# Optimization experiments

Hardware: AMD Instinct MI355X
Metric: run time of the kernel (lower is better)

The kernel has to match this reference:

```python
import jax, jax.numpy as jnp
import numpy as np

IN_DIM, H_DIM, OUT_DIM, N_LAYERS = 512, 1024, 512, 2


def _linear_params(key, out_d, in_d, bias=True):
    k1, k2 = jax.random.split(key)
    bound = 1.0 / np.sqrt(in_d)
    W = jax.random.uniform(k1, (out_d, in_d), jnp.float32, -bound, bound)
    if bias:
        b = jax.random.uniform(k2, (out_d,), jnp.float32, -bound, bound)
        return W, b
    return (W,)


def setup_inputs() -> dict:
    key = jax.random.key(0)
    keys = jax.random.split(key, 32)
    inp = {"x": jax.random.normal(keys[0], (32, 512, IN_DIM), jnp.float32)}
    ki = 1
    for layer in range(N_LAYERS):
        lin = IN_DIM if layer == 0 else H_DIM
        for gate in ("z", "r", "g"):
            W, b = _linear_params(keys[ki], H_DIM, lin); ki += 1
            inp[f"Wx{gate}{layer}"] = W
            inp[f"bx{gate}{layer}"] = b
            (Wh,) = _linear_params(keys[ki], H_DIM, H_DIM, bias=False); ki += 1
            inp[f"Wh{gate}{layer}"] = Wh
    Why, bhy = _linear_params(keys[ki], OUT_DIM, H_DIM)
    inp["Why"] = Why
    inp["bhy"] = bhy
    return inp


def _gru_forward(x, layers, Why, bhy):
    B = x.shape[0]
    h0 = tuple(jnp.zeros((B, H_DIM), x.dtype) for _ in range(N_LAYERS))

    def cell(p, h_prev, xin):
        Wxz, bxz, Whz, Wxr, bxr, Whr, Wxg, bxg, Whg = p
        z = jax.nn.sigmoid(xin @ Wxz.T + bxz + h_prev @ Whz.T)
        r = jax.nn.sigmoid(xin @ Wxr.T + bxr + h_prev @ Whr.T)
        g = jnp.tanh(xin @ Wxg.T + bxg + (r * h_prev) @ Whg.T)
        return z * h_prev + (1.0 - z) * g

    def step(hs, xt):
        cur = xt
        new_hs = []
        for p, h in zip(layers, hs):
            h_new = cell(p, h, cur)
            new_hs.append(h_new)
            cur = h_new
        yt = cur @ Why.T + bhy  # (B, O)
        return tuple(new_hs), yt

    xs = jnp.swapaxes(x, 0, 1)  # (S, B, I)
    final_hs, ys = jax.lax.scan(step, h0, xs)
    layer_output = jnp.swapaxes(ys, 0, 1)  # (B, S, O)
    hidden_state = jnp.stack(final_hs, axis=1)  # (B, L, H)
    return layer_output, hidden_state


def reference(x,
              Wxz0, bxz0, Whz0, Wxr0, bxr0, Whr0, Wxg0, bxg0, Whg0,
              Wxz1, bxz1, Whz1, Wxr1, bxr1, Whr1, Wxg1, bxg1, Whg1,
              Why, bhy):
    layers = [
        (Wxz0, bxz0, Whz0, Wxr0, bxr0, Whr0, Wxg0, bxg0, Whg0),
        (Wxz1, bxz1, Whz1, Wxr1, bxr1, Whr1, Wxg1, bxg1, Whg1),
    ]
    return _gru_forward(x, layers, Why, bhy)
```

## Files before the change

### kernel.cpp

```cpp
#include <hip/hip_runtime.h>

#define SS 512
#define NWG 52
#define NTHR 512
#define OUT_HID_OFF 8388608

typedef _Float16 fh8 __attribute__((ext_vector_type(8)));
typedef float f32x4 __attribute__((ext_vector_type(4)));

struct GP {
  const float *x;
  const float *Wxz0,*bxz0,*Whz0,*Wxr0,*bxr0,*Whr0,*Wxg0,*bxg0,*Whg0;
  const float *Wxz1,*bxz1,*Whz1,*Wxr1,*bxr1,*Whr1,*Wxg1,*bxg1,*Whg1;
  const float *Why,*bhy;
  float *out;
  _Float16 *xb;
  _Float16 *wzr0,*wzr1,*wg0,*wg1,*wy;
  float *h0f,*h1f;
  _Float16 *h0h,*h1h;
  float *z0,*z1;
  _Float16 *r0,*r1;
  unsigned *fg0,*fg1;
  unsigned *fzr0,*fzr1;
  unsigned *fy;
};

__device__ __forceinline__ void astore(float* p, float v) {
  __hip_atomic_store(p, v, __ATOMIC_RELAXED, __HIP_MEMORY_SCOPE_AGENT);
}
__device__ __forceinline__ void bload(uint4& d, const void* p) {
  asm volatile("global_load_dwordx4 %0, %1, off sc0 sc1"
               : "=&v"(d) : "v"(p) : "memory");
}
__device__ __forceinline__ void bload1(float& d, const float* p) {
  asm volatile("global_load_dword %0, %1, off sc0 sc1"
               : "=&v"(d) : "v"(p) : "memory");
}
__device__ __forceinline__ void sstore(_Float16* pd, float v) {
  _Float16 h = (_Float16)v;
  unsigned short u; __builtin_memcpy(&u, &h, 2);
  asm volatile("global_store_short %0, %1, off sc0 sc1"
               :: "v"(pd), "v"((unsigned)u) : "memory");
}
__device__ __forceinline__ fh8 u2h(uint4 v){ fh8 r; __builtin_memcpy(&r, &v, 16); return r; }
__device__ __forceinline__ uint4 h2u(fh8 v){ uint4 r; __builtin_memcpy(&r, &v, 16); return r; }
__device__ __forceinline__ float sigmf(float v){ return 1.f/(1.f+__expf(-v)); }

__global__ __launch_bounds__(256) void pack(GP p) {
  const long gid = (long)blockIdx.x*256 + threadIdx.x;
  if (gid < 1441792) {
    long u; int KC; _Float16* dst;
    if (gid < 393216)       { u=gid;         KC=48; dst=p.wzr0; }
    else if (gid < 917504)  { u=gid-393216;  KC=64; dst=p.wzr1; }
    else if (gid < 1114112) { u=gid-917504;  KC=48; dst=p.wg0;  }
    else if (gid < 1376256) { u=gid-1114112; KC=64; dst=p.wg1;  }
    else                    { u=gid-1376256; KC=32; dst=p.wy;   }
    const int per = KC*64;
    const int ntg = (int)(u/per); const int r = (int)(u%per);
    const int kc = r>>6, lane = r&63;
    const int n = ntg*16 + (lane&15);
    const int k = kc*32 + ((lane>>4)<<3);
    const float* src;
    if (gid < 393216) {
      int g = n>>10, nn = n&1023;
      src = (k<512) ? ((g?p.Wxr0:p.Wxz0) + (size_t)nn*512 + k)
                    : ((g?p.Whr0:p.Whz0) + (size_t)nn*1024 + (k-512));
    } else if (gid < 917504) {
      int g = n>>10, nn = n&1023;
      src = (k<1024) ? ((g?p.Wxr1:p.Wxz1) + (size_t)nn*1024 + k)
                     : ((g?p.Whr1:p.Whz1) + (size_t)nn*1024 + (k-1024));
    } else if (gid < 1114112) {
      src = (k<512) ? (p.Wxg0 + (size_t)n*512 + k)
                    : (p.Whg0 + (size_t)n*1024 + (k-512));
    } else if (gid < 1376256) {
      src = (k<1024) ? (p.Wxg1 + (size_t)n*1024 + k)
                     : (p.Whg1 + (size_t)n*1024 + (k-1024));
    } else {
      src = p.Why + (size_t)n*1024 + k;
    }
    float4 f0 = *(const float4*)src, f1 = *(const float4*)(src+4);
    fh8 h;
    h[0]=(_Float16)f0.x; h[1]=(_Float16)f0.y; h[2]=(_Float16)f0.z; h[3]=(_Float16)f0.w;
    h[4]=(_Float16)f1.x; h[5]=(_Float16)f1.y; h[6]=(_Float16)f1.z; h[7]=(_Float16)f1.w;
    *(fh8*)(dst + u*8) = h;
  } else if (gid < 2490368) {
    const long e = (gid - 1441792)*8;
    float4 f0 = *(const float4*)(p.x + e), f1 = *(const float4*)(p.x + e + 4);
    fh8 h;
    h[0]=(_Float16)f0.x; h[1]=(_Float16)f0.y; h[2]=(_Float16)f0.z; h[3]=(_Float16)f0.w;
    h[4]=(_Float16)f1.x; h[5]=(_Float16)f1.y; h[6]=(_Float16)f1.z; h[7]=(_Float16)f1.w;
    *(fh8*)(p.xb + e) = h;
  }
}

__device__ __forceinline__ void waitf(const unsigned* fb, int n, int need) {
  if (need > 0) {
    if ((int)threadIdx.x < n) {
      const unsigned* f = fb + (size_t)threadIdx.x*32;
      while ((int)__hip_atomic_load(f, __ATOMIC_RELAXED, __HIP_MEMORY_SCOPE_AGENT) < need)
        __builtin_amdgcn_s_sleep(1);
    }
    asm volatile("" ::: "memory");
    __syncthreads();
  }
}
__device__ __forceinline__ void setflag(unsigned* f, unsigned v) {
  asm volatile("s_waitcnt vmcnt(0) lgkmcnt(0)" ::: "memory");
  __syncthreads();
  if (threadIdx.x == 0)
    __hip_atomic_store(f, v, __ATOMIC_RELAXED, __HIP_MEMORY_SCOPE_AGENT);
}

__device__ __forceinline__ void issue_copy(uint4* R, const _Float16* base, int row, int s16) {
  const char* sp = (const char*)(base + (size_t)row*1024) + s16*64;
  bload(R[0], sp); bload(R[1], sp+16); bload(R[2], sp+32); bload(R[3], sp+48);
}
__device__ __forceinline__ void issue_prod(uint4* Ra, uint4* Rh,
    const _Float16* ra, const _Float16* ha, int row, int s16) {
  const char* rp = (const char*)(ra + (size_t)row*1024) + s16*64;
  const char* hp = (const char*)(ha + (size_t)row*1024) + s16*64;
  #pragma unroll
  for (int q = 0; q < 4; ++q) { bload(Ra[q], rp + q*16); bload(Rh[q], hp + q*16); }
}
__device__ __forceinline__ void issue_x(uint4* R, const _Float16* xab, int row, int s16) {
  const uint4* sp = (const uint4*)(xab + (size_t)row*262144 + (size_t)s16*32);
  R[0]=sp[0]; R[1]=sp[1]; R[2]=sp[2]; R[3]=sp[3];
}
__device__ __forceinline__ void commit4(const uint4* R, char* As, int s, int row, int s16) {
  const int key = (row & 15) << 4;
  char* d = As + (size_t)row*4096;
  const int kb0 = s*1024 + s16*64;
  #pragma unroll
  for (int q = 0; q < 4; ++q) *(uint4*)(d + ((kb0 + q*16) ^ key)) = R[q];
}
__device__ __forceinline__ void commit_prod(const uint4* Ra, const uint4* Rh,
    char* As, int s, int row, int s16) {
  const int key = (row & 15) << 4;
  char* d = As + (size_t)row*4096;
  const int kb0 = s*1024 + s16*64;
  #pragma unroll
  for (int q = 0; q < 4; ++q) {
    fh8 o = u2h(Ra[q]) * u2h(Rh[q]);
    *(uint4*)(d + ((kb0 + q*16) ^ key)) = h2u(o);
  }
}

__device__ __forceinline__ void sweep_range(const char* As, const _Float16* wpk,
    int ntg, int KC, int k0, int k1, int l, f32x4& acc0, f32x4& acc1) {
  const int lrow = l & 15, key = lrow << 4, lg16 = (l >> 4) << 4;
  const char* ab = As + (size_t)lrow*4096;
  const _Float16* wb = wpk + (size_t)ntg*KC*512 + (size_t)l*8;
  #pragma unroll 8
  for (int kk = k0; kk < k1; ++kk) {
    const int off = (kk*64 + lg16) ^ key;
    fh8 a0 = *(const fh8*)(ab + off);
    fh8 a1 = *(const fh8*)(ab + 16*4096 + off);
    fh8 b  = *(const fh8*)(wb + (size_t)kk*512);
    acc0 = __builtin_amdgcn_mfma_f32_16x16x32_f16(a0, b, acc0, 0, 0, 0);
    acc1 = __builtin_amdgcn_mfma_f32_16x16x32_f16(a1, b, acc1, 0, 0, 0);
  }
}

__device__ __forceinline__ void epi_zr(const f32x4& a0, const f32x4& a1, int ntg, int l,
    const float* bz, const float* br, float* zbuf, _Float16* rbuf) {
  const int col = (ntg << 4) | (l & 15);
  const int gate = col >> 10, cc = col & 1023;
  const float bias = gate ? br[cc] : bz[cc];
  const int brow = (l >> 4) << 2;
  #pragma unroll
  for (int q = 0; q < 4; ++q) {
    const float v0 = sigmf(a0[q]+bias), v1 = sigmf(a1[q]+bias);
    if (gate) {
      sstore(rbuf + (size_t)(brow+q)*1024 + cc, v0);
      sstore(rbuf + (size_t)(brow+q+16)*1024 + cc, v1);
    } else {
      astore(zbuf + (size_t)(brow+q)*1024 + cc, v0);
      astore(zbuf + (size_t)(brow+q+16)*1024 + cc, v1);
    }
  }
}

__global__ __launch_bounds__(NTHR, 2) void gru_main(GP p) {
  __shared__ char As[131072];
  const int tid = threadIdx.x, wg = blockIdx.x;
  const int wid = tid >> 6, l = tid & 63;
  const int row = tid >> 4, s16 = tid & 15;
  const int brow = (l >> 4) << 2;

  if (wg < 16) {
    const int ntg = wg*8 + wid;
    for (int t = 0; t < SS; ++t) {
      { uint4 Rx[4];
        issue_x(Rx, p.xb + (size_t)t*512, row, s16);
        commit4(Rx, As, 0, row, s16); }
      __syncthreads();
      f32x4 a0 = {0.f,0.f,0.f,0.f}, a1 = {0.f,0.f,0.f,0.f};
      sweep_range(As, p.wzr0, ntg, 48, 0, 16, l, a0, a1);
      waitf(p.fg0, 8, t);
      { const _Float16* hb = p.h0h + (size_t)((t-1)&3)*32768;
        uint4 R0[4], R1[4];
        issue_copy(R0, hb, row, s16);
        issue_copy(R1, hb+512, row, s16);
        asm volatile("s_waitcnt vmcnt(0)" ::: "memory");
        __builtin_amdgcn_sched_barrier(0);
        commit4(R0, As, 1, row, s16);
        commit4(R1, As, 2, row, s16); }
      __syncthreads();
      sweep_range(As, p.wzr0, ntg, 48, 16, 48, l, a0, a1);
      epi_zr(a0, a1, ntg, l, p.bxz0, p.bxr0,
             p.z0 + (size_t)(t&1)*32768, p.r0 + (size_t)(t&1)*32768);
      setflag(p.fzr0 + (size_t)wg*32, (unsigned)(t+1));
    }
  } else if (wg < 32) {
    const int ntg = (wg-16)*8 + wid;
    for (int t = 0; t < SS; ++t) {
      waitf(p.fg0, 8, t+1);
      { const _Float16* hb = p.h0h + (size_t)(t&3)*32768;
        uint4 R0[4], R1[4];
        issue_copy(R0, hb, row, s16);
        issue_copy(R1, hb+512, row, s16);
        asm volatile("s_waitcnt vmcnt(0)" ::: "memory");
        __builtin_amdgcn_sched_barrier(0);
        commit4(R0, As, 0, row, s16);
        commit4(R1, As, 1, row, s16); }
      __syncthreads();
      f32x4 a0 = {0.f,0.f,0.f,0.f}, a1 = {0.f,0.f,0.f,0.f};
      sweep_range(As, p.wzr1, ntg, 64, 0, 32, l, a0, a1);
      waitf(p.fg1, 8, t);
      { const _Float16* hb = p.h1h + (size_t)((t-1)&3)*32768;
        uint4 R0[4], R1[4];
        issue_copy(R0, hb, row, s16);
        issue_copy(R1, hb+512, row, s16);
        asm volatile("s_waitcnt vmcnt(0)" ::: "memory");
        __builtin_amdgcn_sched_barrier(0);
        commit4(R0, As, 2, row, s16);
        commit4(R1, As, 3, row, s16); }
      __syncthreads();
      sweep_range(As, p.wzr1, ntg, 64, 32, 64, l, a0, a1);
      epi_zr(a0, a1, ntg, l, p.bxz1, p.bxr1,
             p.z1 + (size_t)(t&1)*32768, p.r1 + (size_t)(t&1)*32768);
      setflag(p.fzr1 + (size_t)(wg-16)*32, (unsigned)(t+1));
    }
  } else if (wg < 40) {
    const int gi = wg - 32;
    const int ntg = gi*8 + wid;
    const int colB = (ntg << 4) | (l & 15);
    const float biasB = p.bxg0[colB];
    float hv[8];
    #pragma unroll
    for (int q = 0; q < 8; ++q) hv[q] = 0.f;
    for (int u = 0; u < SS; ++u) {
      { uint4 Rx[4];
        issue_x(Rx, p.xb + (size_t)u*512, row, s16);
        commit4(Rx, As, 0, row, s16); }
      __syncthreads();
      f32x4 a0 = {0.f,0.f,0.f,0.f}, a1 = {0.f,0.f,0.f,0.f};
      sweep_range(As, p.wg0, ntg, 48, 0, 16, l, a0, a1);
      waitf(p.fzr0, 16, u+1);
      waitf(p.fg0,  8,  u);
      waitf(p.fzr1, 16, u-3);
      waitf(p.fg1,  8,  u-3);
      { const float*    zr = p.z0 + (size_t)(u&1)*32768;
        const _Float16* rr = p.r0 + (size_t)(u&1)*32768;
        const _Float16* hh = p.h0h + (size_t)((u-1)&3)*32768;
        float zv[8];
        uint4 Ra[8], Rh[8];
        issue_prod(&Ra[0], &Rh[0], rr, hh, row, s16);
        issue_prod(&Ra[4], &Rh[4], rr+512, hh+512, row, s16);
        #pragma unroll
        for (int q = 0; q < 4; ++q) {
          bload1(zv[q],   zr + (size_t)(brow+q)*1024 + colB);
          bload1(zv[4+q], zr + (size_t)(brow+q+16)*1024 + colB);
        }
        asm volatile("s_waitcnt vmcnt(0)" ::: "memory");
        __builtin_amdgcn_sched_barrier(0);
        commit_prod(&Ra[0], &Rh[0], As, 1, row, s16);
        commit_prod(&Ra[4], &Rh[4], As, 2, row, s16);
        __syncthreads();
        sweep_range(As, p.wg0, ntg, 48, 16, 48, l, a0, a1);
        float* hF = p.h0f + (size_t)(u&3)*32768;
        _Float16* hH = p.h0h + (size_t)(u&3)*32768;
        #pragma unroll
        for (int q = 0; q < 4; ++q) {
          { const float g = tanhf(a0[q]+biasB);
            const float hn = zv[q]*hv[q] + (1.f-zv[q])*g;
            hv[q] = hn;
            astore(hF + (size_t)(brow+q)*1024 + colB, hn);
            sstore(hH + (size_t)(brow+q)*1024 + colB, hn); }
          { const float g = tanhf(a1[q]+biasB);
            const float hn = zv[4+q]*hv[4+q] + (1.f-zv[4+q])*g;
            hv[4+q] = hn;
            astore(hF + (size_t)(brow+q+16)*1024 + colB, hn);
            sstore(hH + (size_t)(brow+q+16)*1024 + colB, hn); }
        }
      }
      setflag(p.fg0 + (size_t)gi*32, (unsigned)(u+1));
    }
    #pragma unroll
    for (int q = 0; q < 4; ++q) {
      p.out[OUT_HID_OFF + (size_t)(brow+q)*2048 + colB]    = hv[q];
      p.out[OUT_HID_OFF + (size_t)(brow+q+16)*2048 + colB] = hv[4+q];
    }
  } else if (wg < 48) {
    const int gi = wg - 40;
    const int ntg = gi*8 + wid;
    const int colB = (ntg << 4) | (l & 15);
    const float biasB = p.bxg1[colB];
    float hv[8];
    #pragma unroll
    for (int q = 0; q < 8; ++q) hv[q] = 0.f;
    for (int v = 0; v < SS; ++v) {
      waitf(p.fg0, 8, v+1);
      { const _Float16* hb = p.h0h + (size_t)(v&3)*32768;
        uint4 R0[4], R1[4];
        issue_copy(R0, hb, row, s16);
        issue_copy(R1, hb+512, row, s16);
        asm volatile("s_waitcnt vmcnt(0)" ::: "memory");
        __builtin_amdgcn_sched_barrier(0);
        commit4(R0, As, 0, row, s16);
        commit4(R1, As, 1, row, s16); }
      __syncthreads();
      f32x4 a0 = {0.f,0.f,0.f,0.f}, a1 = {0.f,0.f,0.f,0.f};
      sweep_range(As, p.wg1, ntg, 64, 0, 32, l, a0, a1);
      waitf(p.fzr1, 16, v+1);
      waitf(p.fg1,  8,  v);
      waitf(p.fy,   4,  v-3);
      { const float*    zr = p.z1 + (size_t)(v&1)*32768;
        const _Float16* rr = p.r1 + (size_t)(v&1)*32768;
        const _Float16* hh = p.h1h + (size_t)((v-1)&3)*32768;
        float zv[8];
        uint4 Ra[8], Rh[8];
        issue_prod(&Ra[0], &Rh[0], rr, hh, row, s16);
        issue_prod(&Ra[4], &Rh[4], rr+512, hh+512, row, s16);
        #pragma unroll
        for (int q = 0; q < 4; ++q) {
          bload1(zv[q],   zr + (size_t)(brow+q)*1024 + colB);
          bload1(zv[4+q], zr + (size_t)(brow+q+16)*1024 + colB);
        }
        asm volatile("s_waitcnt vmcnt(0)" ::: "memory");
        __builtin_amdgcn_sched_barrier(0);
        commit_prod(&Ra[0], &Rh[0], As, 2, row, s16);
        commit_prod(&Ra[4], &Rh[4], As, 3, row, s16);
        __syncthreads();
        sweep_range(As, p.wg1, ntg, 64, 32, 64, l, a0, a1);
        float* hF = p.h1f + (size_t)(v&3)*32768;
        _Float16* hH = p.h1h + (size_t)(v&3)*32768;
        #pragma unroll
        for (int q = 0; q < 4; ++q) {
          { const float g = tanhf(a0[q]+biasB);
            const float hn = zv[q]*hv[q] + (1.f-zv[q])*g;
            hv[q] = hn;
            astore(hF + (size_t)(brow+q)*1024 + colB, hn);
            sstore(hH + (size_t)(brow+q)*1024 + colB, hn); }
          { const float g = tanhf(a1[q]+biasB);
            const float hn = zv[4+q]*hv[4+q] + (1.f-zv[4+q])*g;
            hv[4+q] = hn;
            astore(hF + (size_t)(brow+q+16)*1024 + colB, hn);
            sstore(hH + (size_t)(brow+q+16)*1024 + colB, hn); }
        }
      }
      setflag(p.fg1 + (size_t)gi*32, (unsigned)(v+1));
    }
    #pragma unroll
    for (int q = 0; q < 4; ++q) {
      p.out[OUT_HID_OFF + (size_t)(brow+q)*2048 + 1024 + colB]    = hv[q];
      p.out[OUT_HID_OFF + (size_t)(brow+q+16)*2048 + 1024 + colB] = hv[4+q];
    }
  } else {
    const int ntg = (wg-48)*8 + wid;
    const int col = (ntg << 4) | (l & 15);
    const float bias = p.bhy[col];
    for (int w = 0; w < SS; ++w) {
      waitf(p.fg1, 8, w+1);
      { const _Float16* hb = p.h1h + (size_t)(w&3)*32768;
        uint4 R0[4], R1[4];
        issue_copy(R0, hb, row, s16);
        issue_copy(R1, hb+512, row, s16);
        asm volatile("s_waitcnt vmcnt(0)" ::: "memory");
        __builtin_amdgcn_sched_barrier(0);
        commit4(R0, As, 0, row, s16);
        commit4(R1, As, 1, row, s16); }
      __syncthreads();
      f32x4 a0 = {0.f,0.f,0.f,0.f}, a1 = {0.f,0.f,0.f,0.f};
      sweep_range(As, p.wy, ntg, 32, 0, 32, l, a0, a1);
      #pragma unroll
      for (int q = 0; q < 4; ++q) {
        p.out[(size_t)(brow+q)*262144    + (size_t)w*512 + col] = a0[q] + bias;
        p.out[(size_t)(brow+q+16)*262144 + (size_t)w*512 + col] = a1[q] + bias;
      }
      setflag(p.fy + (size_t)(wg-48)*32, (unsigned)(w+1));
    }
  }
}

extern "C" void kernel_launch(void* const* d_in, const int* in_sizes, int n_in,
                              void* d_out, int out_size, void* d_ws, size_t ws_size,
                              hipStream_t stream) {
  GP P;
  P.x    = (const float*)d_in[0];
  P.Wxz0 = (const float*)d_in[1];  P.bxz0 = (const float*)d_in[2];  P.Whz0 = (const float*)d_in[3];
  P.Wxr0 = (const float*)d_in[4];  P.bxr0 = (const float*)d_in[5];  P.Whr0 = (const float*)d_in[6];
  P.Wxg0 = (const float*)d_in[7];  P.bxg0 = (const float*)d_in[8];  P.Whg0 = (const float*)d_in[9];
  P.Wxz1 = (const float*)d_in[10]; P.bxz1 = (const float*)d_in[11]; P.Whz1 = (const float*)d_in[12];
  P.Wxr1 = (const float*)d_in[13]; P.bxr1 = (const float*)d_in[14]; P.Whr1 = (const float*)d_in[15];
  P.Wxg1 = (const float*)d_in[16]; P.bxg1 = (const float*)d_in[17]; P.Whg1 = (const float*)d_in[18];
  P.Why  = (const float*)d_in[19]; P.bhy  = (const float*)d_in[20];
  P.out  = (float*)d_out;

  char* ws = (char*)d_ws;
  P.xb   = (_Float16*)(ws + 0);
  P.wzr0 = (_Float16*)(ws + 16777216);
  P.wzr1 = (_Float16*)(ws + 23068672);
  P.wg0  = (_Float16*)(ws + 31457280);
  P.wg1  = (_Float16*)(ws + 34603008);
  P.wy   = (_Float16*)(ws + 38797312);
  P.h0f  = (float*)   (ws + 39845888);
  P.h1f  = (float*)   (ws + 40370176);
  P.h0h  = (_Float16*)(ws + 40894464);
  P.h1h  = (_Float16*)(ws + 41156608);
  P.z0   = (float*)   (ws + 41418752);
  P.z1   = (float*)   (ws + 41680896);
  P.r0   = (_Float16*)(ws + 41943040);
  P.r1   = (_Float16*)(ws + 42074112);
  P.fg0  = (unsigned*)(ws + 42205184);
  P.fg1  = (unsigned*)(ws + 42206208);
  P.fzr0 = (unsigned*)(ws + 42207232);
  P.fzr1 = (unsigned*)(ws + 42209280);
  P.fy   = (unsigned*)(ws + 42211328);

  hipMemsetAsync(ws + 39845888, 0, 42213888 - 39845888, stream);

  pack<<<dim3(9728), dim3(256), 0, stream>>>(P);

  void* args[] = { &P };
  hipError_t err = hipLaunchCooperativeKernel((const void*)gru_main,
                                              dim3(NWG), dim3(NTHR), args, 0, stream);
  if (err != hipSuccess) {
    (void)hipGetLastError();
    gru_main<<<dim3(NWG), dim3(NTHR), 0, stream>>>(P);
  }
}
```

Measured before the change: 7.825 ms.

## Split recurrent GRU work across 100 workgroups with half-batch tiles and paired stores

Each workgroup now handles 4 column tiles. Each wave computes a 16-row half of the batch instead of both halves, so the zr and g stages use twice as many workgroups (NWG goes from 52 to 100). Per-element fp16 and fp32 stores are replaced by lane-pair shuffles and 32/64-bit atomic stores, and multiple flag waits are merged into one concurrent poll. The aim is to shorten the per-timestep critical path by spreading the MFMA sweeps over more CUs, at the cost of more flags to poll and more cross-workgroup synchronization.

```diff
diff --git a/kernel.cpp b/kernel.cpp
--- a/kernel.cpp
+++ b/kernel.cpp
@@ -1,7 +1,7 @@
 #include <hip/hip_runtime.h>
 
 #define SS 512
-#define NWG 52
+#define NWG 100
 #define NTHR 512
 #define OUT_HID_OFF 8388608
 
@@ -25,7 +25,16 @@
   unsigned *fy;
 };
 
-__device__ __forceinline__ void astore(float* p, float v) {
+__device__ __forceinline__ void astoref(float* p, float v) {
+  __hip_atomic_store(p, v, __ATOMIC_RELAXED, __HIP_MEMORY_SCOPE_AGENT);
+}
+__device__ __forceinline__ void astore2f(float* p, float a, float b) {
+  unsigned long long u;
+  float t[2] = {a, b};
+  __builtin_memcpy(&u, t, 8);
+  __hip_atomic_store((unsigned long long*)p, u, __ATOMIC_RELAXED, __HIP_MEMORY_SCOPE_AGENT);
+}
+__device__ __forceinline__ void astoreu(unsigned* p, unsigned v) {
   __hip_atomic_store(p, v, __ATOMIC_RELAXED, __HIP_MEMORY_SCOPE_AGENT);
 }
 __device__ __forceinline__ void bload(uint4& d, const void* p) {
@@ -36,15 +45,16 @@
   asm volatile("global_load_dword %0, %1, off sc0 sc1"
                : "=&v"(d) : "v"(p) : "memory");
 }
-__device__ __forceinline__ void sstore(_Float16* pd, float v) {
-  _Float16 h = (_Float16)v;
-  unsigned short u; __builtin_memcpy(&u, &h, 2);
-  asm volatile("global_store_short %0, %1, off sc0 sc1"
-               :: "v"(pd), "v"((unsigned)u) : "memory");
-}
 __device__ __forceinline__ fh8 u2h(uint4 v){ fh8 r; __builtin_memcpy(&r, &v, 16); return r; }
 __device__ __forceinline__ uint4 h2u(fh8 v){ uint4 r; __builtin_memcpy(&r, &v, 16); return r; }
 __device__ __forceinline__ float sigmf(float v){ return 1.f/(1.f+__expf(-v)); }
+__device__ __forceinline__ unsigned pkpair(float v) {
+  float o = __shfl_xor(v, 1, 64);
+  _Float16 ha = (_Float16)v, hb = (_Float16)o;
+  unsigned short ua, ub;
+  __builtin_memcpy(&ua,&ha,2); __builtin_memcpy(&ub,&hb,2);
+  return (unsigned)ua | ((unsigned)ub << 16);
+}
 
 __global__ __launch_bounds__(256) void pack(GP p) {
   const long gid = (long)blockIdx.x*256 + threadIdx.x;
@@ -93,13 +103,15 @@
   }
 }
 
+__device__ __forceinline__ void pollone(const unsigned* f, int need) {
+  if (f && need > 0)
+    while ((int)__hip_atomic_load(f, __ATOMIC_RELAXED, __HIP_MEMORY_SCOPE_AGENT) < need)
+      __builtin_amdgcn_s_sleep(1);
+}
 __device__ __forceinline__ void waitf(const unsigned* fb, int n, int need) {
   if (need > 0) {
-    if ((int)threadIdx.x < n) {
-      const unsigned* f = fb + (size_t)threadIdx.x*32;
-      while ((int)__hip_atomic_load(f, __ATOMIC_RELAXED, __HIP_MEMORY_SCOPE_AGENT) < need)
-        __builtin_amdgcn_s_sleep(1);
-    }
+    if ((int)threadIdx.x < n)
+      pollone(fb + (size_t)threadIdx.x*32, need);
     asm volatile("" ::: "memory");
     __syncthreads();
   }
@@ -145,6 +157,19 @@
   }
 }
 
+__device__ __forceinline__ void sweep_half(const char* As, const _Float16* wpk,
+    int ntg, int KC, int k0, int k1, int l, int half, f32x4& acc) {
+  const int lrow = l & 15, key = lrow << 4, lg16 = (l >> 4) << 4;
+  const char* ab = As + (size_t)lrow*4096 + (size_t)half*16*4096;
+  const _Float16* wb = wpk + (size_t)ntg*KC*512 + (size_t)l*8;
+  #pragma unroll 8
+  for (int kk = k0; kk < k1; ++kk) {
+    const int off = (kk*64 + lg16) ^ key;
+    fh8 a = *(const fh8*)(ab + off);
+    fh8 b = *(const fh8*)(wb + (size_t)kk*512);
+    acc = __builtin_amdgcn_mfma_f32_16x16x32_f16(a, b, acc, 0, 0, 0);
+  }
+}
 __device__ __forceinline__ void sweep_range(const char* As, const _Float16* wpk,
     int ntg, int KC, int k0, int k1, int l, f32x4& acc0, f32x4& acc1) {
   const int lrow = l & 15, key = lrow << 4, lg16 = (l >> 4) << 4;
@@ -161,21 +186,21 @@
   }
 }
 
-__device__ __forceinline__ void epi_zr(const f32x4& a0, const f32x4& a1, int ntg, int l,
+__device__ __forceinline__ void epi_zr_p(const f32x4& a, int tile, int half, int l,
     const float* bz, const float* br, float* zbuf, _Float16* rbuf) {
-  const int col = (ntg << 4) | (l & 15);
+  const int col = (tile << 4) | (l & 15);
   const int gate = col >> 10, cc = col & 1023;
   const float bias = gate ? br[cc] : bz[cc];
-  const int brow = (l >> 4) << 2;
+  const int r0 = half*16 + ((l >> 4) << 2);
   #pragma unroll
   for (int q = 0; q < 4; ++q) {
-    const float v0 = sigmf(a0[q]+bias), v1 = sigmf(a1[q]+bias);
+    const float v = sigmf(a[q] + bias);
     if (gate) {
-      sstore(rbuf + (size_t)(brow+q)*1024 + cc, v0);
-      sstore(rbuf + (size_t)(brow+q+16)*1024 + cc, v1);
+      unsigned w = pkpair(v);
+      if (!(l & 1)) astoreu((unsigned*)(rbuf + (size_t)(r0+q)*1024 + cc), w);
     } else {
-      astore(zbuf + (size_t)(brow+q)*1024 + cc, v0);
-      astore(zbuf + (size_t)(brow+q+16)*1024 + cc, v1);
+      float o = __shfl_xor(v, 1, 64);
+      if (!(l & 1)) astore2f(zbuf + (size_t)(r0+q)*1024 + cc, v, o);
     }
   }
 }
@@ -185,18 +210,18 @@
   const int tid = threadIdx.x, wg = blockIdx.x;
   const int wid = tid >> 6, l = tid & 63;
   const int row = tid >> 4, s16 = tid & 15;
-  const int brow = (l >> 4) << 2;
-
-  if (wg < 16) {
-    const int ntg = wg*8 + wid;
+  const int half = wid >> 2;
+
+  if (wg < 32) {
+    const int tile = wg*4 + (wid & 3);
     for (int t = 0; t < SS; ++t) {
       { uint4 Rx[4];
         issue_x(Rx, p.xb + (size_t)t*512, row, s16);
         commit4(Rx, As, 0, row, s16); }
       __syncthreads();
-      f32x4 a0 = {0.f,0.f,0.f,0.f}, a1 = {0.f,0.f,0.f,0.f};
-      sweep_range(As, p.wzr0, ntg, 48, 0, 16, l, a0, a1);
-      waitf(p.fg0, 8, t);
+      f32x4 a = {0.f,0.f,0.f,0.f};
+      sweep_half(As, p.wzr0, tile, 48, 0, 16, l, half, a);
+      waitf(p.fg0, 16, t);
       { const _Float16* hb = p.h0h + (size_t)((t-1)&3)*32768;
         uint4 R0[4], R1[4];
         issue_copy(R0, hb, row, s16);
@@ -206,15 +231,15 @@
         commit4(R0, As, 1, row, s16);
         commit4(R1, As, 2, row, s16); }
       __syncthreads();
-      sweep_range(As, p.wzr0, ntg, 48, 16, 48, l, a0, a1);
-      epi_zr(a0, a1, ntg, l, p.bxz0, p.bxr0,
-             p.z0 + (size_t)(t&1)*32768, p.r0 + (size_t)(t&1)*32768);
+      sweep_half(As, p.wzr0, tile, 48, 16, 48, l, half, a);
+      epi_zr_p(a, tile, half, l, p.bxz0, p.bxr0,
+               p.z0 + (size_t)(t&1)*32768, p.r0 + (size_t)(t&1)*32768);
       setflag(p.fzr0 + (size_t)wg*32, (unsigned)(t+1));
     }
-  } else if (wg < 32) {
-    const int ntg = (wg-16)*8 + wid;
+  } else if (wg < 64) {
+    const int tile = (wg-32)*4 + (wid & 3);
     for (int t = 0; t < SS; ++t) {
-      waitf(p.fg0, 8, t+1);
+      waitf(p.fg0, 16, t+1);
       { const _Float16* hb = p.h0h + (size_t)(t&3)*32768;
         uint4 R0[4], R1[4];
         issue_copy(R0, hb, row, s16);
@@ -224,9 +249,9 @@
         commit4(R0, As, 0, row, s16);
         commit4(R1, As, 1, row, s16); }
       __syncthreads();
-      f32x4 a0 = {0.f,0.f,0.f,0.f}, a1 = {0.f,0.f,0.f,0.f};
-      sweep_range(As, p.wzr1, ntg, 64, 0, 32, l, a0, a1);
-      waitf(p.fg1, 8, t);
+      f32x4 a = {0.f,0.f,0.f,0.f};
+      sweep_half(As, p.wzr1, tile, 64, 0, 32, l, half, a);
+      waitf(p.fg1, 16, t);
       { const _Float16* hb = p.h1h + (size_t)((t-1)&3)*32768;
         uint4 R0[4], R1[4];
         issue_copy(R0, hb, row, s16);
@@ -236,81 +261,78 @@
         commit4(R0, As, 2, row, s16);
         commit4(R1, As, 3, row, s16); }
       __syncthreads();
-      sweep_range(As, p.wzr1, ntg, 64, 32, 64, l, a0, a1);
-      epi_zr(a0, a1, ntg, l, p.bxz1, p.bxr1,
-             p.z1 + (size_t)(t&1)*32768, p.r1 + (size_t)(t&1)*32768);
-      setflag(p.fzr1 + (size_t)(wg-16)*32, (unsigned)(t+1));
-    }
-  } else if (wg < 40) {
-    const int gi = wg - 32;
-    const int ntg = gi*8 + wid;
-    const int colB = (ntg << 4) | (l & 15);
+      sweep_half(As, p.wzr1, tile, 64, 32, 64, l, half, a);
+      epi_zr_p(a, tile, half, l, p.bxz1, p.bxr1,
+               p.z1 + (size_t)(t&1)*32768, p.r1 + (size_t)(t&1)*32768);
+      setflag(p.fzr1 + (size_t)(wg-32)*32, (unsigned)(t+1));
+    }
+  } else if (wg < 80) {
+    const int gi = wg - 64;
+    const int tile = gi*4 + (wid & 3);
+    const int colB = (tile << 4) | (l & 15);
+    const int r0 = half*16 + ((l >> 4) << 2);
     const float biasB = p.bxg0[colB];
-    float hv[8];
-    #pragma unroll
-    for (int q = 0; q < 8; ++q) hv[q] = 0.f;
+    float hv[4] = {0.f,0.f,0.f,0.f};
     for (int u = 0; u < SS; ++u) {
       { uint4 Rx[4];
         issue_x(Rx, p.xb + (size_t)u*512, row, s16);
         commit4(Rx, As, 0, row, s16); }
       __syncthreads();
-      f32x4 a0 = {0.f,0.f,0.f,0.f}, a1 = {0.f,0.f,0.f,0.f};
-      sweep_range(As, p.wg0, ntg, 48, 0, 16, l, a0, a1);
-      waitf(p.fzr0, 16, u+1);
-      waitf(p.fg0,  8,  u);
-      waitf(p.fzr1, 16, u-3);
-      waitf(p.fg1,  8,  u-3);
+      f32x4 a = {0.f,0.f,0.f,0.f};
+      sweep_half(As, p.wg0, tile, 48, 0, 16, l, half, a);
+      { const unsigned* f = nullptr; int need = 0;
+        if (tid < 32)      { f = p.fzr0 + (size_t)tid*32;      need = u+1; }
+        else if (tid < 48) { f = p.fg0  + (size_t)(tid-32)*32; need = u;   }
+        else if (tid < 80) { f = p.fzr1 + (size_t)(tid-48)*32; need = u-3; }
+        else if (tid < 96) { f = p.fg1  + (size_t)(tid-80)*32; need = u-3; }
+        pollone(f, need);
+        asm volatile("" ::: "memory");
+        __syncthreads(); }
       { const float*    zr = p.z0 + (size_t)(u&1)*32768;
         const _Float16* rr = p.r0 + (size_t)(u&1)*32768;
         const _Float16* hh = p.h0h + (size_t)((u-1)&3)*32768;
-        float zv[8];
+        float zv[4];
         uint4 Ra[8], Rh[8];
         issue_prod(&Ra[0], &Rh[0], rr, hh, row, s16);
         issue_prod(&Ra[4], &Rh[4], rr+512, hh+512, row, s16);
         #pragma unroll
-        for (int q = 0; q < 4; ++q) {
-          bload1(zv[q],   zr + (size_t)(brow+q)*1024 + colB);
-          bload1(zv[4+q], zr + (size_t)(brow+q+16)*1024 + colB);
-        }
+        for (int q = 0; q < 4; ++q)
+          bload1(zv[q], zr + (size_t)(r0+q)*1024 + colB);
         asm volatile("s_waitcnt vmcnt(0)" ::: "memory");
         __builtin_amdgcn_sched_barrier(0);
         commit_prod(&Ra[0], &Rh[0], As, 1, row, s16);
         commit_prod(&Ra[4], &Rh[4], As, 2, row, s16);
         __syncthreads();
-        sweep_range(As, p.wg0, ntg, 48, 16, 48, l, a0, a1);
+        sweep_half(As, p.wg0, tile, 48, 16, 48, l, half, a);
         float* hF = p.h0f + (size_t)(u&3)*32768;
         _Float16* hH = p.h0h + (size_t)(u&3)*32768;
         #pragma unroll
         for (int q = 0; q < 4; ++q) {
-          { const float g = tanhf(a0[q]+biasB);
-            const float hn = zv[q]*hv[q] + (1.f-zv[q])*g;
-            hv[q] = hn;
-            astore(hF + (size_t)(brow+q)*1024 + colB, hn);
-            sstore(hH + (size_t)(brow+q)*1024 + colB, hn); }
-          { const float g = tanhf(a1[q]+biasB);
-            const float hn = zv[4+q]*hv[4+q] + (1.f-zv[4+q])*g;
-            hv[4+q] = hn;
-            astore(hF + (size_t)(brow+q+16)*1024 + colB, hn);
-            sstore(hH + (size_t)(brow+q+16)*1024 + colB, hn); }
+          const float g = tanhf(a[q] + biasB);
+          const float hn = zv[q]*hv[q] + (1.f - zv[q])*g;
+          hv[q] = hn;
+          float o = __shfl_xor(hn, 1, 64);
+          unsigned w = pkpair(hn);
+          if (!(l & 1)) {
+            astore2f(hF + (size_t)(r0+q)*1024 + colB, hn, o);
+            astoreu((unsigned*)(hH + (size_t)(r0+q)*1024 + colB), w);
+          }
         }
       }
       setflag(p.fg0 + (size_t)gi*32, (unsigned)(u+1));
     }
     #pragma unroll
-    for (int q = 0; q < 4; ++q) {
-      p.out[OUT_HID_OFF + (size_t)(brow+q)*2048 + colB]    = hv[q];
-      p.out[OUT_HID_OFF + (size_t)(brow+q+16)*2048 + colB] = hv[4+q];
-    }
-  } else if (wg < 48) {
-    const int gi = wg - 40;
-    const int ntg = gi*8 + wid;
-    const int colB = (ntg << 4) | (l & 15);
+    for (int q = 0; q < 4; ++q)
+      p.out[OUT_HID_OFF + (size_t)(r0+q)*2048 + colB] = hv[q];
+  } else if (wg < 96) {
+    const int gi = wg - 80;
+    const int tile = gi*4 + (wid & 3);
+    const int colB = (tile << 4) | (l & 15);
+    const int r0 = half*16 + ((l >> 4) << 2);
     const float biasB = p.bxg1[colB];
-    float hv[8];
-    #pragma unroll
-    for (int q = 0; q < 8; ++q) hv[q] = 0.f;
+    float hv[4] = {0.f,0.f,0.f,0.f};
     for (int v = 0; v < SS; ++v) {
-      waitf(p.fg0, 8, v+1);
+      waitf(p.fg0, 16, v+1);
       { const _Float16* hb = p.h0h + (size_t)(v&3)*32768;
         uint4 R0[4], R1[4];
         issue_copy(R0, hb, row, s16);
@@ -320,58 +342,58 @@
         commit4(R0, As, 0, row, s16);
         commit4(R1, As, 1, row, s16); }
       __syncthreads();
-      f32x4 a0 = {0.f,0.f,0.f,0.f}, a1 = {0.f,0.f,0.f,0.f};
-      sweep_range(As, p.wg1, ntg, 64, 0, 32, l, a0, a1);
-      waitf(p.fzr1, 16, v+1);
-      waitf(p.fg1,  8,  v);
-      waitf(p.fy,   4,  v-3);
+      f32x4 a = {0.f,0.f,0.f,0.f};
+      sweep_half(As, p.wg1, tile, 64, 0, 32, l, half, a);
+      { const unsigned* f = nullptr; int need = 0;
+        if (tid < 32)      { f = p.fzr1 + (size_t)tid*32;      need = v+1; }
+        else if (tid < 48) { f = p.fg1  + (size_t)(tid-32)*32; need = v;   }
+        else if (tid < 52) { f = p.fy   + (size_t)(tid-48)*32; need = v-3; }
+        pollone(f, need);
+        asm volatile("" ::: "memory");
+        __syncthreads(); }
       { const float*    zr = p.z1 + (size_t)(v&1)*32768;
         const _Float16* rr = p.r1 + (size_t)(v&1)*32768;
         const _Float16* hh = p.h1h + (size_t)((v-1)&3)*32768;
-        float zv[8];
+        float zv[4];
         uint4 Ra[8], Rh[8];
         issue_prod(&Ra[0], &Rh[0], rr, hh, row, s16);
         issue_prod(&Ra[4], &Rh[4], rr+512, hh+512, row, s16);
         #pragma unroll
-        for (int q = 0; q < 4; ++q) {
-          bload1(zv[q],   zr + (size_t)(brow+q)*1024 + colB);
-          bload1(zv[4+q], zr + (size_t)(brow+q+16)*1024 + colB);
-        }
+        for (int q = 0; q < 4; ++q)
+          bload1(zv[q], zr + (size_t)(r0+q)*1024 + colB);
         asm volatile("s_waitcnt vmcnt(0)" ::: "memory");
         __builtin_amdgcn_sched_barrier(0);
         commit_prod(&Ra[0], &Rh[0], As, 2, row, s16);
         commit_prod(&Ra[4], &Rh[4], As, 3, row, s16);
         __syncthreads();
-        sweep_range(As, p.wg1, ntg, 64, 32, 64, l, a0, a1);
+        sweep_half(As, p.wg1, tile, 64, 32, 64, l, half, a);
         float* hF = p.h1f + (size_t)(v&3)*32768;
         _Float16* hH = p.h1h + (size_t)(v&3)*32768;
         #pragma unroll
         for (int q = 0; q < 4; ++q) {
-          { const float g = tanhf(a0[q]+biasB);
-            const float hn = zv[q]*hv[q] + (1.f-zv[q])*g;
-            hv[q] = hn;
-            astore(hF + (size_t)(brow+q)*1024 + colB, hn);
-            sstore(hH + (size_t)(brow+q)*1024 + colB, hn); }
-          { const float g = tanhf(a1[q]+biasB);
-            const float hn = zv[4+q]*hv[4+q] + (1.f-zv[4+q])*g;
-            hv[4+q] = hn;
-            astore(hF + (size_t)(brow+q+16)*1024 + colB, hn);
-            sstore(hH + (size_t)(brow+q+16)*1024 + colB, hn); }
+          const float g = tanhf(a[q] + biasB);
+          const float hn = zv[q]*hv[q] + (1.f - zv[q])*g;
+          hv[q] = hn;
+          float o = __shfl_xor(hn, 1, 64);
+          unsigned w = pkpair(hn);
+          if (!(l & 1)) {
+            astore2f(hF + (size_t)(r0+q)*1024 + colB, hn, o);
+            astoreu((unsigned*)(hH + (size_t)(r0+q)*1024 + colB), w);
+          }
         }
       }
       setflag(p.fg1 + (size_t)gi*32, (unsigned)(v+1));
     }
     #pragma unroll
-    for (int q = 0; q < 4; ++q) {
-      p.out[OUT_HID_OFF + (size_t)(brow+q)*2048 + 1024 + colB]    = hv[q];
-      p.out[OUT_HID_OFF + (size_t)(brow+q+16)*2048 + 1024 + colB] = hv[4+q];
-    }
+    for (int q = 0; q < 4; ++q)
+      p.out[OUT_HID_OFF + (size_t)(r0+q)*2048 + 1024 + colB] = hv[q];
   } else {
-    const int ntg = (wg-48)*8 + wid;
+    const int ntg = (wg-96)*8 + wid;
     const int col = (ntg << 4) | (l & 15);
+    const int brow = (l >> 4) << 2;
     const float bias = p.bhy[col];
     for (int w = 0; w < SS; ++w) {
-      waitf(p.fg1, 8, w+1);
+      waitf(p.fg1, 16, w+1);
       { const _Float16* hb = p.h1h + (size_t)(w&3)*32768;
         uint4 R0[4], R1[4];
         issue_copy(R0, hb, row, s16);
@@ -388,7 +410,7 @@
         p.out[(size_t)(brow+q)*262144    + (size_t)w*512 + col] = a0[q] + bias;
         p.out[(size_t)(brow+q+16)*262144 + (size_t)w*512 + col] = a1[q] + bias;
       }
-      setflag(p.fy + (size_t)(wg-48)*32, (unsigned)(w+1));
+      setflag(p.fy + (size_t)(wg-96)*32, (unsigned)(w+1));
     }
   }
 }
@@ -423,12 +445,12 @@
   P.r0   = (_Float16*)(ws + 41943040);
   P.r1   = (_Float16*)(ws + 42074112);
   P.fg0  = (unsigned*)(ws + 42205184);
-  P.fg1  = (unsigned*)(ws + 42206208);
-  P.fzr0 = (unsigned*)(ws + 42207232);
-  P.fzr1 = (unsigned*)(ws + 42209280);
-  P.fy   = (unsigned*)(ws + 42211328);
-
-  hipMemsetAsync(ws + 39845888, 0, 42213888 - 39845888, stream);
+  P.fg1  = (unsigned*)(ws + 42207232);
+  P.fzr0 = (unsigned*)(ws + 42209280);
+  P.fzr1 = (unsigned*)(ws + 42213376);
+  P.fy   = (unsigned*)(ws + 42217472);
+
+  hipMemsetAsync(ws + 39845888, 0, 42217984 - 39845888, stream);
 
   pack<<<dim3(9728), dim3(256), 0, stream>>>(P);
 
```

Result: no change. 7.936 ms (+1.4%).
